# Optimization experiments

Hardware: AMD Instinct MI355X
Metric: run time of the kernel (lower is better)

## Reference

```python
import jax, jax.numpy as jnp
import numpy as np

DIM = 180
HEADS = 6
NSQ = 12          # num_gs_seed_sqrt
N = NSQ * NSQ     # 144 tokens per window
B = 2048


def _relative_position_index(nsq: int) -> np.ndarray:
    coords = np.stack(np.meshgrid(np.arange(nsq), np.arange(nsq), indexing='ij'))  # [2,nsq,nsq]
    flat = coords.reshape(2, -1)                       # [2, N]
    rel = flat[:, :, None] - flat[:, None, :]          # [2, N, N]
    rel = rel.transpose(1, 2, 0)                       # [N, N, 2]
    rel[:, :, 0] += nsq - 1
    rel[:, :, 1] += nsq - 1
    rel[:, :, 0] *= 2 * nsq - 1
    return rel.sum(-1)                                 # [N, N] int

REL_IDX = jnp.asarray(_relative_position_index(NSQ))


def setup_inputs() -> dict:
    key = jax.random.key(0)
    ks = jax.random.split(key, 10)
    d = DIM
    std_lin = 1.0 / np.sqrt(d)
    inp = {
        'gs': jax.random.normal(ks[0], (B, N, d), dtype=jnp.float32),
        'wq': jax.random.normal(ks[1], (d, d), dtype=jnp.float32) * std_lin,
        'bq': jnp.zeros((d,), jnp.float32),
        'wk': jax.random.normal(ks[2], (d, d), dtype=jnp.float32) * std_lin,
        'bk': jnp.zeros((d,), jnp.float32),
        'wv': jax.random.normal(ks[3], (d, d), dtype=jnp.float32) * std_lin,
        'bv': jnp.zeros((d,), jnp.float32),
        'wp': jax.random.normal(ks[4], (d, d), dtype=jnp.float32) * std_lin,
        'bp': jnp.zeros((d,), jnp.float32),
        # trunc_normal(std=0.02) table: [(2*nsq-1)^2, heads]
        'bias_table': jax.random.normal(ks[5], ((2 * NSQ - 1) ** 2, HEADS), dtype=jnp.float32) * 0.02,
    }
    return inp


def reference(gs, wq, bq, wk, bk, wv, bv, wp, bp, bias_table):
    b, n, c = gs.shape
    h = HEADS
    hd = c // h
    scale = hd ** -0.5

    def heads(x, w, bias):
        y = x @ w + bias                                  # [b, n, c]
        return y.reshape(b, n, h, hd).transpose(0, 2, 1, 3)  # [b, h, n, hd]

    q = heads(gs, wq, bq) * scale
    k = heads(gs, wk, bk)
    v = heads(gs, wv, bv)

    attn = jnp.einsum('bhqd,bhkd->bhqk', q, k)            # [b, h, n, n]
    rel_bias = bias_table[REL_IDX]                        # [n, n, h]
    attn = attn + rel_bias.transpose(2, 0, 1)[None]       # + [1, h, n, n]
    attn = jax.nn.softmax(attn, axis=-1)

    out = jnp.einsum('bhqk,bhkd->bhqd', attn, v)          # [b, h, n, hd]
    out = out.transpose(0, 2, 1, 3).reshape(b, n, c)
    return out @ wp + bp
```

## Files before the change

### kernel.cpp

```cpp
#include <hip/hip_runtime.h>


typedef __bf16 bf16_t;
typedef __bf16 bf16x8 __attribute__((ext_vector_type(8)));
typedef __bf16 bf16x4 __attribute__((ext_vector_type(4)));
typedef float f32x4 __attribute__((ext_vector_type(4)));

#define MFMA16(a, b, c) __builtin_amdgcn_mfma_f32_16x16x32_bf16((a), (b), (c), 0, 0, 0)

static __device__ __forceinline__ f32x4 fzero4() {
    f32x4 z; z[0] = 0.f; z[1] = 0.f; z[2] = 0.f; z[3] = 0.f; return z;
}
static __device__ __forceinline__ bf16x8 bzero8() {
    bf16x8 z;
    #pragma unroll
    for (int i = 0; i < 8; ++i) z[i] = (bf16_t)0.f;
    return z;
}

__global__ void pack_kernel(const float* __restrict__ wq, const float* __restrict__ bq,
                            const float* __restrict__ wk, const float* __restrict__ bk,
                            const float* __restrict__ wv, const float* __restrict__ bv,
                            const float* __restrict__ wp, const float* __restrict__ bt,
                            bf16_t* __restrict__ Wqkv, bf16_t* __restrict__ Wp,
                            bf16_t* __restrict__ BIASf, float* __restrict__ bqkv)
{
    const int t = blockIdx.x * blockDim.x + threadIdx.x;
    const int stride = gridDim.x * blockDim.x;
    const float L2E = 1.4426950408889634f;
    const float qscale = 0.18257418583505536f * L2E;

    for (int i = t; i < 6 * 6 * 6 * 512; i += stride) {
        int j = i & 7, lane = (i >> 3) & 63;
        int f = i >> 9;
        int nt = f % 6, kt = (f / 6) % 6, h = f / 36;
        int kin = kt * 32 + (lane >> 4) * 8 + j;
        int c = nt * 16 + (lane & 15);
        int sec = c >> 5, d = c & 31;
        float v = 0.f;
        if (kin < 180 && d < 30) {
            int col = h * 30 + d;
            if (sec == 0)      v = wq[kin * 180 + col] * qscale;
            else if (sec == 1) v = wk[kin * 180 + col];
            else               v = wv[kin * 180 + col];
        }
        Wqkv[i] = (bf16_t)v;
    }
    for (int i = t; i < 2 * 6 * 6 * 512; i += stride) {
        int j = i & 7, lane = (i >> 3) & 63;
        int f = i >> 9;
        int ntl = f % 6, kt = (f / 6) % 6, half = f / 36;
        int nt = half * 6 + ntl;
        int kin = kt * 32 + (lane >> 4) * 8 + j;
        int hh = kin >> 5, d = kin & 31;
        int cout = nt * 16 + (lane & 15);
        float v = 0.f;
        if (d < 30 && cout < 180) v = wp[(hh * 30 + d) * 180 + cout];
        Wp[i] = (bf16_t)v;
    }
    for (int i = t; i < 6 * 9 * 9 * 64; i += stride) {
        int lane = i & 63;
        int f = i >> 6;
        int nt = f % 9, wvq = (f / 9) % 9, h = f / 81;
        int q = wvq * 16 + (lane & 15);
        int qi = q / 12, qj = q % 12;
        #pragma unroll
        for (int r = 0; r < 4; ++r) {
            int k = nt * 16 + (lane >> 4) * 4 + r;
            int ki = k / 12, kj = k % 12;
            int rel = (qi - ki + 11) * 23 + (qj - kj + 11);
            BIASf[i * 4 + r] = (bf16_t)(bt[rel * 6 + h] * L2E);
        }
    }
    for (int i = t; i < 576; i += stride) {
        int c = i % 96, h = i / 96;
        int sec = c >> 5, d = c & 31;
        float v = 0.f;
        if (d < 30) {
            if (sec == 0)      v = bq[h * 30 + d] * qscale;
            else if (sec == 1) v = bk[h * 30 + d];
            else               v = bv[h * 30 + d];
        }
        bqkv[i] = v;
    }
}

__global__ __launch_bounds__(576, 2)
void attn_kernel(const float* __restrict__ gs,
                 const bf16_t* __restrict__ Wqkv, const bf16_t* __restrict__ Wp,
                 const bf16_t* __restrict__ BIASf, const float* __restrict__ bqkv,
                 const float* __restrict__ bp, float* __restrict__ out)
{
    __shared__ __align__(16) unsigned char smem[133632];

    const int tid = threadIdx.x;
    const int lane = tid & 63;
    const int wv = tid >> 6;
    const int l15 = lane & 15;
    const int lg = lane >> 4;
    const int win = blockIdx.x;
    const float* __restrict__ gsw = gs + (size_t)win * 25920;

    constexpr int WB0     = 0;
    constexpr int WB1     = 36864;
    constexpr int ST_BASE = 73728;
    constexpr int K_BASE  = 115200;
    constexpr int VT_BASE = 124416;

    int4 wld[4];
    #pragma unroll
    for (int i = 0; i < 4; ++i)
        wld[i] = *(const int4*)((const char*)Wqkv + (tid + i * 576) * 16);

    bf16x8 xa[6];
    {
        const int row = wv * 16 + l15;
        const float4* __restrict__ g4 = (const float4*)(gsw + row * 180);
        #pragma unroll
        for (int kt = 0; kt < 6; ++kt) {
            const int c0 = kt * 32 + lg * 8;
            float4 lo = {0.f, 0.f, 0.f, 0.f}, hi = {0.f, 0.f, 0.f, 0.f};
            if (c0 + 4 <= 180) lo = g4[c0 >> 2];
            if (c0 + 8 <= 180) hi = g4[(c0 >> 2) + 1];
            bf16x8 v;
            v[0] = (bf16_t)lo.x; v[1] = (bf16_t)lo.y; v[2] = (bf16_t)lo.z; v[3] = (bf16_t)lo.w;
            v[4] = (bf16_t)hi.x; v[5] = (bf16_t)hi.y; v[6] = (bf16_t)hi.z; v[7] = (bf16_t)hi.w;
            xa[kt] = v;
        }
    }
    #pragma unroll
    for (int i = 0; i < 4; ++i)
        *(int4*)(smem + WB0 + (tid + i * 576) * 16) = wld[i];
    __syncthreads();

    bf16x8 ao[6];
    char* const pb = (char*)smem + ST_BASE + wv * 4608;
    const int pswz = (l15 & 6) << 3;

    #pragma unroll
    for (int h = 0; h < 6; ++h) {
        const int WCUR = (h & 1) ? WB1 : WB0;
        const int WNXT = (h & 1) ? WB0 : WB1;

        f32x4 acc[6];
        #pragma unroll
        for (int nt = 0; nt < 6; ++nt) acc[nt] = fzero4();
        __builtin_amdgcn_s_setprio(1);
        #pragma unroll
        for (int kt = 0; kt < 6; ++kt) {
            #pragma unroll
            for (int nt = 0; nt < 6; ++nt) {
                bf16x8 bw = *(const bf16x8*)(smem + WCUR + ((kt * 6 + nt) * 64 + lane) * 16);
                acc[nt] = MFMA16(xa[kt], bw, acc[nt]);
            }
        }
        __builtin_amdgcn_s_setprio(0);

        bf16_t q8[8];
        {
            const int row0 = wv * 16 + lg * 4;
            #pragma unroll
            for (int nt = 0; nt < 6; ++nt) {
                const float bias = bqkv[h * 96 + nt * 16 + l15];
                const int sec = nt >> 1;
                const int d32 = ((nt & 1) << 4) + l15;
                const int vswz = (wv < 8) ? (((d32 >> 2) & 3) << 4) : 0;
                #pragma unroll
                for (int r = 0; r < 4; ++r) {
                    const int rr = row0 + r;
                    const bf16_t bvl = (bf16_t)(acc[nt][r] + bias);
                    if (sec == 0)
                        q8[(nt & 1) * 4 + r] = bvl;
                    else if (sec == 1)
                        *(bf16_t*)(smem + K_BASE + rr * 64 + ((d32 * 2) ^ ((rr & 6) << 3))) = bvl;
                    else
                        *(bf16_t*)(smem + VT_BASE + d32 * 288 + ((rr * 2) ^ vswz)) = bvl;
                }
            }
        }
        __syncthreads();

        int4 wn[4];
        {
            const char* __restrict__ nsrc =
                (h < 5) ? ((const char*)Wqkv + (h + 1) * 36864) : (const char*)Wp;
            #pragma unroll
            for (int i = 0; i < 4; ++i)
                wn[i] = *(const int4*)(nsrc + (tid + i * 576) * 16);
        }

        #pragma unroll
        for (int r = 0; r < 4; ++r) {
            const int row = lg * 4 + r;
            const int swz = (row & 6) << 3;
            *(bf16_t*)(pb + row * 64 + ((l15 * 2) ^ swz))      = q8[r];
            *(bf16_t*)(pb + row * 64 + ((l15 * 2 + 32) ^ swz)) = q8[4 + r];
        }
        asm volatile("" ::: "memory");
        bf16x8 aq = *(const bf16x8*)(pb + l15 * 64 + ((lg * 16) ^ ((l15 & 6) << 3)));
        asm volatile("" ::: "memory");

        float sum = 0.f;
        #pragma unroll
        for (int nt = 0; nt < 9; ++nt) {
            const int krow = nt * 16 + l15;
            bf16x8 kf = *(const bf16x8*)(smem + K_BASE + krow * 64 +
                                         ((lg * 16) ^ ((krow & 6) << 3)));
            f32x4 sv = MFMA16(kf, aq, fzero4());
            bf16x4 b4 = *(const bf16x4*)(BIASf +
                        (size_t)((((h * 9 + wv) * 9 + nt) * 64 + lane) * 4));
            bf16x4 pw;
            #pragma unroll
            for (int r = 0; r < 4; ++r) {
                float p = exp2f(sv[r] + (float)b4[r]);
                sum += p;
                pw[r] = (bf16_t)p;
            }
            if (nt < 8)
                *(bf16x4*)(pb + (nt >> 1) * 1024 + l15 * 64 +
                           ((((nt & 1) << 5) + lg * 8) ^ pswz)) = pw;
            else
                *(bf16x4*)(pb + 4096 + l15 * 32 + lg * 8) = pw;
        }
        sum += __shfl_xor(sum, 16, 64);
        sum += __shfl_xor(sum, 32, 64);
        const float rinv = 1.f / sum;
        asm volatile("" ::: "memory");

        f32x4 o0 = fzero4(), o1 = fzero4();
        __builtin_amdgcn_s_setprio(1);
        #pragma unroll
        for (int kt = 0; kt < 4; ++kt) {
            const int vs0 = ((l15 >> 2) & 3) << 4;
            bf16x8 ap  = *(const bf16x8*)(pb + kt * 1024 + l15 * 64 + ((lg * 16) ^ pswz));
            bf16x8 bv0 = *(const bf16x8*)(smem + VT_BASE + l15 * 288 + kt * 64 + ((lg * 16) ^ vs0));
            bf16x8 bv1 = *(const bf16x8*)(smem + VT_BASE + (16 + l15) * 288 + kt * 64 + ((lg * 16) ^ vs0));
            o0 = MFMA16(ap, bv0, o0);
            o1 = MFMA16(ap, bv1, o1);
        }
        {
            bf16x8 ap  = bzero8();
            bf16x8 bv0 = bzero8();
            bf16x8 bv1 = bzero8();
            if (lg < 2) {
                ap  = *(const bf16x8*)(pb + 4096 + l15 * 32 + lg * 16);
                bv0 = *(const bf16x8*)(smem + VT_BASE + l15 * 288 + 256 + lg * 16);
                bv1 = *(const bf16x8*)(smem + VT_BASE + (16 + l15) * 288 + 256 + lg * 16);
            }
            o0 = MFMA16(ap, bv0, o0);
            o1 = MFMA16(ap, bv1, o1);
        }
        __builtin_amdgcn_s_setprio(0);

        #pragma unroll
        for (int i = 0; i < 4; ++i)
            *(int4*)(smem + WNXT + (tid + i * 576) * 16) = wn[i];

        asm volatile("" ::: "memory");
        #pragma unroll
        for (int r = 0; r < 4; ++r) {
            const float rq = __shfl(rinv, lg * 4 + r, 16);
            const int row = lg * 4 + r;
            const int swz = (row & 6) << 3;
            *(bf16_t*)(pb + row * 64 + ((l15 * 2) ^ swz))      = (bf16_t)(o0[r] * rq);
            *(bf16_t*)(pb + row * 64 + ((l15 * 2 + 32) ^ swz)) = (bf16_t)(o1[r] * rq);
        }
        asm volatile("" ::: "memory");
        ao[h] = *(const bf16x8*)(pb + l15 * 64 + ((lg * 16) ^ ((l15 & 6) << 3)));

        __syncthreads();
    }

    float* __restrict__ og = out + (size_t)win * 25920;
    int4 wp1[4];
    #pragma unroll
    for (int i = 0; i < 4; ++i)
        wp1[i] = *(const int4*)((const char*)Wp + 36864 + (tid + i * 576) * 16);

    #pragma unroll
    for (int half = 0; half < 2; ++half) {
        const int WH = half ? WB1 : WB0;
        f32x4 accp[6];
        #pragma unroll
        for (int nt = 0; nt < 6; ++nt) accp[nt] = fzero4();
        __builtin_amdgcn_s_setprio(1);
        #pragma unroll
        for (int kt = 0; kt < 6; ++kt) {
            #pragma unroll
            for (int nt = 0; nt < 6; ++nt) {
                bf16x8 bw = *(const bf16x8*)(smem + WH + ((kt * 6 + nt) * 64 + lane) * 16);
                accp[nt] = MFMA16(ao[kt], bw, accp[nt]);
            }
        }
        __builtin_amdgcn_s_setprio(0);
        #pragma unroll
        for (int nt = 0; nt < 6; ++nt) {
            const int col = half * 96 + nt * 16 + l15;
            if (col < 180) {
                const float bias = bp[col];
                #pragma unroll
                for (int r = 0; r < 4; ++r) {
                    const int row = wv * 16 + lg * 4 + r;
                    og[row * 180 + col] = accp[nt][r] + bias;
                }
            }
        }
        if (half == 0) {
            #pragma unroll
            for (int i = 0; i < 4; ++i)
                *(int4*)(smem + WB1 + (tid + i * 576) * 16) = wp1[i];
            __syncthreads();
        }
    }
}

extern "C" void kernel_launch(void* const* d_in, const int* in_sizes, int n_in,
                              void* d_out, int out_size, void* d_ws, size_t ws_size,
                              hipStream_t stream) {
    const float* gs = (const float*)d_in[0];
    const float* wq = (const float*)d_in[1];
    const float* bq = (const float*)d_in[2];
    const float* wk = (const float*)d_in[3];
    const float* bk = (const float*)d_in[4];
    const float* wv = (const float*)d_in[5];
    const float* bv = (const float*)d_in[6];
    const float* wp = (const float*)d_in[7];
    const float* bp = (const float*)d_in[8];
    const float* bt = (const float*)d_in[9];

    char* ws = (char*)d_ws;
    bf16_t* Wqkv  = (bf16_t*)(ws);
    bf16_t* Wp    = (bf16_t*)(ws + 221184);
    bf16_t* BIASf = (bf16_t*)(ws + 294912);
    float*  bqkv  = (float*)(ws + 543744);

    pack_kernel<<<256, 256, 0, stream>>>(wq, bq, wk, bk, wv, bv, wp, bt,
                                         Wqkv, Wp, BIASf, bqkv);
    attn_kernel<<<2048, 576, 0, stream>>>(gs, Wqkv, Wp, BIASf, bqkv, bp, (float*)d_out);
}
```

Before: 344.3 us.

## Read weight fragments directly from global/L2 instead of staging in LDS

Removes the double-buffered LDS staging of QKV and projection weights. The MFMA B-operands are now loaded straight from global memory, relying on L1/L2 caching because every block reads the same weights. This shrinks shared memory from about 130KB to about 78KB. K and V^T are double-buffered by head parity, which lets the trailing per-head barrier go, and the V^T write is vectorized to bf16x4. The trade-off is per-MFMA global load latency in the projection loops in exchange for fewer barriers and less LDS traffic.

```diff
diff --git a/kernel.cpp b/kernel.cpp
--- a/kernel.cpp
+++ b/kernel.cpp
@@ -91,7 +91,7 @@
                  const bf16_t* __restrict__ BIASf, const float* __restrict__ bqkv,
                  const float* __restrict__ bp, float* __restrict__ out)
 {
-    __shared__ __align__(16) unsigned char smem[133632];
+    __shared__ __align__(16) unsigned char smem[78336];
 
     const int tid = threadIdx.x;
     const int lane = tid & 63;
@@ -101,16 +101,9 @@
     const int win = blockIdx.x;
     const float* __restrict__ gsw = gs + (size_t)win * 25920;
 
-    constexpr int WB0     = 0;
-    constexpr int WB1     = 36864;
-    constexpr int ST_BASE = 73728;
-    constexpr int K_BASE  = 115200;
-    constexpr int VT_BASE = 124416;
-
-    int4 wld[4];
-    #pragma unroll
-    for (int i = 0; i < 4; ++i)
-        wld[i] = *(const int4*)((const char*)Wqkv + (tid + i * 576) * 16);
+    constexpr int ST_BASE = 0;
+    constexpr int K_BASE  = 41472;
+    constexpr int VT_BASE = 59904;
 
     bf16x8 xa[6];
     {
@@ -128,10 +121,6 @@
             xa[kt] = v;
         }
     }
-    #pragma unroll
-    for (int i = 0; i < 4; ++i)
-        *(int4*)(smem + WB0 + (tid + i * 576) * 16) = wld[i];
-    __syncthreads();
 
     bf16x8 ao[6];
     char* const pb = (char*)smem + ST_BASE + wv * 4608;
@@ -139,9 +128,10 @@
 
     #pragma unroll
     for (int h = 0; h < 6; ++h) {
-        const int WCUR = (h & 1) ? WB1 : WB0;
-        const int WNXT = (h & 1) ? WB0 : WB1;
-
+        const int KB = K_BASE + (h & 1) * 9216;
+        const int VB = VT_BASE + (h & 1) * 9216;
+
+        const bf16_t* __restrict__ wsrc = Wqkv + h * 18432;
         f32x4 acc[6];
         #pragma unroll
         for (int nt = 0; nt < 6; ++nt) acc[nt] = fzero4();
@@ -150,7 +140,7 @@
         for (int kt = 0; kt < 6; ++kt) {
             #pragma unroll
             for (int nt = 0; nt < 6; ++nt) {
-                bf16x8 bw = *(const bf16x8*)(smem + WCUR + ((kt * 6 + nt) * 64 + lane) * 16);
+                bf16x8 bw = *(const bf16x8*)(wsrc + (size_t)((kt * 6 + nt) * 64 + lane) * 8);
                 acc[nt] = MFMA16(xa[kt], bw, acc[nt]);
             }
         }
@@ -160,34 +150,36 @@
         {
             const int row0 = wv * 16 + lg * 4;
             #pragma unroll
-            for (int nt = 0; nt < 6; ++nt) {
+            for (int nt = 0; nt < 2; ++nt) {
                 const float bias = bqkv[h * 96 + nt * 16 + l15];
-                const int sec = nt >> 1;
+                #pragma unroll
+                for (int r = 0; r < 4; ++r)
+                    q8[nt * 4 + r] = (bf16_t)(acc[nt][r] + bias);
+            }
+            #pragma unroll
+            for (int nt = 2; nt < 4; ++nt) {
+                const float bias = bqkv[h * 96 + nt * 16 + l15];
                 const int d32 = ((nt & 1) << 4) + l15;
-                const int vswz = (wv < 8) ? (((d32 >> 2) & 3) << 4) : 0;
                 #pragma unroll
                 for (int r = 0; r < 4; ++r) {
                     const int rr = row0 + r;
-                    const bf16_t bvl = (bf16_t)(acc[nt][r] + bias);
-                    if (sec == 0)
-                        q8[(nt & 1) * 4 + r] = bvl;
-                    else if (sec == 1)
-                        *(bf16_t*)(smem + K_BASE + rr * 64 + ((d32 * 2) ^ ((rr & 6) << 3))) = bvl;
-                    else
-                        *(bf16_t*)(smem + VT_BASE + d32 * 288 + ((rr * 2) ^ vswz)) = bvl;
+                    *(bf16_t*)(smem + KB + rr * 64 + ((d32 * 2) ^ ((rr & 6) << 3))) =
+                        (bf16_t)(acc[nt][r] + bias);
                 }
             }
+            #pragma unroll
+            for (int nt = 4; nt < 6; ++nt) {
+                const float bias = bqkv[h * 96 + nt * 16 + l15];
+                const int d32 = ((nt & 1) << 4) + l15;
+                const int vswz = (wv < 8) ? (((d32 >> 2) & 3) << 4) : 0;
+                bf16x4 vvv;
+                #pragma unroll
+                for (int r = 0; r < 4; ++r)
+                    vvv[r] = (bf16_t)(acc[nt][r] + bias);
+                *(bf16x4*)(smem + VB + d32 * 288 + ((row0 * 2) ^ vswz)) = vvv;
+            }
         }
         __syncthreads();
-
-        int4 wn[4];
-        {
-            const char* __restrict__ nsrc =
-                (h < 5) ? ((const char*)Wqkv + (h + 1) * 36864) : (const char*)Wp;
-            #pragma unroll
-            for (int i = 0; i < 4; ++i)
-                wn[i] = *(const int4*)(nsrc + (tid + i * 576) * 16);
-        }
 
         #pragma unroll
         for (int r = 0; r < 4; ++r) {
@@ -204,7 +196,7 @@
         #pragma unroll
         for (int nt = 0; nt < 9; ++nt) {
             const int krow = nt * 16 + l15;
-            bf16x8 kf = *(const bf16x8*)(smem + K_BASE + krow * 64 +
+            bf16x8 kf = *(const bf16x8*)(smem + KB + krow * 64 +
                                          ((lg * 16) ^ ((krow & 6) << 3)));
             f32x4 sv = MFMA16(kf, aq, fzero4());
             bf16x4 b4 = *(const bf16x4*)(BIASf +
@@ -233,8 +225,8 @@
         for (int kt = 0; kt < 4; ++kt) {
             const int vs0 = ((l15 >> 2) & 3) << 4;
             bf16x8 ap  = *(const bf16x8*)(pb + kt * 1024 + l15 * 64 + ((lg * 16) ^ pswz));
-            bf16x8 bv0 = *(const bf16x8*)(smem + VT_BASE + l15 * 288 + kt * 64 + ((lg * 16) ^ vs0));
-            bf16x8 bv1 = *(const bf16x8*)(smem + VT_BASE + (16 + l15) * 288 + kt * 64 + ((lg * 16) ^ vs0));
+            bf16x8 bv0 = *(const bf16x8*)(smem + VB + l15 * 288 + kt * 64 + ((lg * 16) ^ vs0));
+            bf16x8 bv1 = *(const bf16x8*)(smem + VB + (16 + l15) * 288 + kt * 64 + ((lg * 16) ^ vs0));
             o0 = MFMA16(ap, bv0, o0);
             o1 = MFMA16(ap, bv1, o1);
         }
@@ -244,17 +236,13 @@
             bf16x8 bv1 = bzero8();
             if (lg < 2) {
                 ap  = *(const bf16x8*)(pb + 4096 + l15 * 32 + lg * 16);
-                bv0 = *(const bf16x8*)(smem + VT_BASE + l15 * 288 + 256 + lg * 16);
-                bv1 = *(const bf16x8*)(smem + VT_BASE + (16 + l15) * 288 + 256 + lg * 16);
+                bv0 = *(const bf16x8*)(smem + VB + l15 * 288 + 256 + lg * 16);
+                bv1 = *(const bf16x8*)(smem + VB + (16 + l15) * 288 + 256 + lg * 16);
             }
             o0 = MFMA16(ap, bv0, o0);
             o1 = MFMA16(ap, bv1, o1);
         }
         __builtin_amdgcn_s_setprio(0);
-
-        #pragma unroll
-        for (int i = 0; i < 4; ++i)
-            *(int4*)(smem + WNXT + (tid + i * 576) * 16) = wn[i];
 
         asm volatile("" ::: "memory");
         #pragma unroll
@@ -267,19 +255,11 @@
         }
         asm volatile("" ::: "memory");
         ao[h] = *(const bf16x8*)(pb + l15 * 64 + ((lg * 16) ^ ((l15 & 6) << 3)));
-
-        __syncthreads();
     }
 
     float* __restrict__ og = out + (size_t)win * 25920;
-    int4 wp1[4];
-    #pragma unroll
-    for (int i = 0; i < 4; ++i)
-        wp1[i] = *(const int4*)((const char*)Wp + 36864 + (tid + i * 576) * 16);
-
     #pragma unroll
     for (int half = 0; half < 2; ++half) {
-        const int WH = half ? WB1 : WB0;
         f32x4 accp[6];
         #pragma unroll
         for (int nt = 0; nt < 6; ++nt) accp[nt] = fzero4();
@@ -288,7 +268,8 @@
         for (int kt = 0; kt < 6; ++kt) {
             #pragma unroll
             for (int nt = 0; nt < 6; ++nt) {
-                bf16x8 bw = *(const bf16x8*)(smem + WH + ((kt * 6 + nt) * 64 + lane) * 16);
+                bf16x8 bw = *(const bf16x8*)(Wp +
+                            (size_t)(((half * 6 + kt) * 6 + nt) * 64 + lane) * 8);
                 accp[nt] = MFMA16(ao[kt], bw, accp[nt]);
             }
         }
@@ -304,12 +285,6 @@
                     og[row * 180 + col] = accp[nt][r] + bias;
                 }
             }
-        }
-        if (half == 0) {
-            #pragma unroll
-            for (int i = 0; i < 4; ++i)
-                *(int4*)(smem + WB1 + (tid + i * 576) * 16) = wp1[i];
-            __syncthreads();
         }
     }
 }
```

Result: slower. 437.5 us (+27.1%).
